# Performance work log

Hardware: AMD Instinct MI355X
Metric: run time of the kernel (lower is better)

## Reference

```python
import jax, jax.numpy as jnp
import numpy as np

B, T, DIM, HEADS = 4, 2048, 1024, 16
D_K = DIM // HEADS


def setup_inputs() -> dict:
    key = jax.random.key(0)
    ks = jax.random.split(key, 5)
    x = jax.random.normal(ks[0], (B, T, DIM), dtype=jnp.float32)
    # nn.Linear params: weight [out, in], bias [out]
    w_qkv = jax.random.normal(ks[1], (3 * DIM, DIM), dtype=jnp.float32) / np.sqrt(DIM)
    b_qkv = jax.random.normal(ks[2], (3 * DIM,), dtype=jnp.float32) * 0.02
    w_out = jax.random.normal(ks[3], (DIM, DIM), dtype=jnp.float32) / np.sqrt(DIM)
    b_out = jax.random.normal(ks[4], (DIM,), dtype=jnp.float32) * 0.02
    # causal mask, broadcast over batch and heads: [1, 1, T, T]
    mask = jnp.tril(jnp.ones((T, T), dtype=jnp.int32))[None, None]
    return {"x": x, "w_qkv": w_qkv, "b_qkv": b_qkv, "w_out": w_out, "b_out": b_out, "mask": mask}


def reference(x, w_qkv, b_qkv, w_out, b_out, mask):
    Bb, Tt, D = x.shape
    # fused QKV projection: [B,T,3D] -> [3,B,H,T,d_k]
    qkv = (x @ w_qkv.T + b_qkv).reshape(Bb, Tt, 3, HEADS, D_K).transpose(2, 0, 3, 1, 4)
    q, k, v = qkv[0], qkv[1], qkv[2]
    scores = jnp.einsum("bhqd,bhkd->bhqk", q, k) / jnp.sqrt(jnp.float32(D_K))
    scores = jnp.where(mask == 0, -jnp.inf, scores)
    attn = jax.nn.softmax(scores, axis=-1)  # [B,H,T,T]
    context = jnp.einsum("bhqk,bhkd->bhqd", attn, v)
    context = context.transpose(0, 2, 1, 3).reshape(Bb, Tt, D)
    return context @ w_out.T + b_out
```

## Files before the change

kernel.cpp:

```cpp
#include <hip/hip_runtime.h>

typedef unsigned short ushort_t;
typedef __bf16 bf16x8 __attribute__((ext_vector_type(8)));
typedef float f32x4 __attribute__((ext_vector_type(4)));

#define BB 4
#define TT 2048
#define DIMD 1024
#define NH 16
#define DK 64
#define MROWS (BB * TT)
#define NQKV (3 * DIMD)

__device__ __forceinline__ ushort_t f2b(float f) {
  __bf16 h = (__bf16)f;
  union { __bf16 h; ushort_t u; } c; c.h = h; return c.u;
}
__device__ __forceinline__ float fexp2(float x) {
  float r;
  asm("v_exp_f32 %0, %1" : "=v"(r) : "v"(x));
  return r;
}

__device__ __forceinline__ void gload_lds16(const void* g, void* l) {
  __builtin_amdgcn_global_load_lds(
      (const __attribute__((address_space(1))) void*)g,
      (__attribute__((address_space(3))) void*)l,
      16, 0, 0);
}

__global__ __launch_bounds__(256) void cast_f32_bf16(
    const float* __restrict__ in, ushort_t* __restrict__ out, int n)
{
  const int i = (blockIdx.x * 256 + threadIdx.x) * 8;
  if (i >= n) return;
  float4 a = *(const float4*)(in + i);
  float4 b = *(const float4*)(in + i + 4);
  ushort_t o[8];
  o[0] = f2b(a.x); o[1] = f2b(a.y); o[2] = f2b(a.z); o[3] = f2b(a.w);
  o[4] = f2b(b.x); o[5] = f2b(b.y); o[6] = f2b(b.z); o[7] = f2b(b.w);
  *(uint4*)(out + i) = *(const uint4*)o;
}

template <bool OUT_F32>
__global__ __launch_bounds__(512, 4) void gemm_bt_pipe(
    const ushort_t* __restrict__ A, const ushort_t* __restrict__ W,
    const float* __restrict__ bias, void* __restrict__ Cp,
    int M, int N, int K)
{
  __shared__ __align__(16) ushort_t As[3][128 * 32];
  __shared__ __align__(16) ushort_t Bs[3][256 * 32];

  const int tid = threadIdx.x;
  const int wave = tid >> 6, lane = tid & 63;
  const int x = blockIdx.x & 7, j = blockIdx.x >> 3;
  const int bm = (x << 3) | (j & 7);
  const int bn = j >> 3;
  const int row0 = bm << 7, col0 = bn << 8;
  const int wm = (wave >> 2) << 6;
  const int wn = (wave & 3) << 6;
  const int fr = lane & 15;
  const int g  = lane >> 4;
  const int g4 = g << 2;
  const int csw = (g ^ (fr >> 2)) << 3;

  const int srow = lane >> 2;
  const int scol = ((lane & 3) ^ ((lane >> 4) & 3)) << 3;
  const int lbase = wave << 9;

  const ushort_t* Ag  = A + (size_t)(row0 + (wave << 4) + srow) * K + scol;
  const ushort_t* Wg0 = W + (size_t)(col0 + (wave << 4) + srow) * K + scol;
  const ushort_t* Wg1 = Wg0 + (size_t)128 * K;

#define STAGE_P(kt, buf)                                                      \
  {                                                                           \
    const size_t _k = (size_t)(kt) << 5;                                      \
    gload_lds16(Ag + _k,  &As[buf][lbase]);                                   \
    gload_lds16(Wg0 + _k, &Bs[buf][lbase]);                                   \
    gload_lds16(Wg1 + _k, &Bs[buf][4096 + lbase]);                            \
  }

  const int NT = K >> 5;
  STAGE_P(0, 0);
  STAGE_P(1, 1);

  f32x4 acc[4][4] = {};
  int cr = 0, st = 2;

  for (int t = 0; t < NT; ++t) {
    if (t + 1 < NT) asm volatile("s_waitcnt vmcnt(3)" ::: "memory");
    else            asm volatile("s_waitcnt vmcnt(0)" ::: "memory");
    __builtin_amdgcn_s_barrier();

    const ushort_t* as_ = As[cr];
    const ushort_t* bs_ = Bs[cr];
    bf16x8 af0 = *(const bf16x8*)&as_[(wm +      fr) * 32 + csw];
    bf16x8 af1 = *(const bf16x8*)&as_[(wm + 16 + fr) * 32 + csw];
    bf16x8 bw0 = *(const bf16x8*)&bs_[(wn +      fr) * 32 + csw];
    bf16x8 bw1 = *(const bf16x8*)&bs_[(wn + 16 + fr) * 32 + csw];
    bf16x8 bw2 = *(const bf16x8*)&bs_[(wn + 32 + fr) * 32 + csw];
    bf16x8 bw3 = *(const bf16x8*)&bs_[(wn + 48 + fr) * 32 + csw];
    if (t + 2 < NT) STAGE_P(t + 2, st);
    asm volatile("s_waitcnt lgkmcnt(0)" ::: "memory");
    __builtin_amdgcn_sched_barrier(0);
    __builtin_amdgcn_s_setprio(1);
    acc[0][0] = __builtin_amdgcn_mfma_f32_16x16x32_bf16(af0, bw0, acc[0][0], 0, 0, 0);
    acc[0][1] = __builtin_amdgcn_mfma_f32_16x16x32_bf16(af0, bw1, acc[0][1], 0, 0, 0);
    acc[0][2] = __builtin_amdgcn_mfma_f32_16x16x32_bf16(af0, bw2, acc[0][2], 0, 0, 0);
    acc[0][3] = __builtin_amdgcn_mfma_f32_16x16x32_bf16(af0, bw3, acc[0][3], 0, 0, 0);
    acc[1][0] = __builtin_amdgcn_mfma_f32_16x16x32_bf16(af1, bw0, acc[1][0], 0, 0, 0);
    acc[1][1] = __builtin_amdgcn_mfma_f32_16x16x32_bf16(af1, bw1, acc[1][1], 0, 0, 0);
    acc[1][2] = __builtin_amdgcn_mfma_f32_16x16x32_bf16(af1, bw2, acc[1][2], 0, 0, 0);
    acc[1][3] = __builtin_amdgcn_mfma_f32_16x16x32_bf16(af1, bw3, acc[1][3], 0, 0, 0);
    __builtin_amdgcn_s_setprio(0);

    bf16x8 af2 = *(const bf16x8*)&as_[(wm + 32 + fr) * 32 + csw];
    bf16x8 af3 = *(const bf16x8*)&as_[(wm + 48 + fr) * 32 + csw];
    asm volatile("s_waitcnt lgkmcnt(0)" ::: "memory");
    __builtin_amdgcn_sched_barrier(0);
    __builtin_amdgcn_s_setprio(1);
    acc[2][0] = __builtin_amdgcn_mfma_f32_16x16x32_bf16(af2, bw0, acc[2][0], 0, 0, 0);
    acc[2][1] = __builtin_amdgcn_mfma_f32_16x16x32_bf16(af2, bw1, acc[2][1], 0, 0, 0);
    acc[2][2] = __builtin_amdgcn_mfma_f32_16x16x32_bf16(af2, bw2, acc[2][2], 0, 0, 0);
    acc[2][3] = __builtin_amdgcn_mfma_f32_16x16x32_bf16(af2, bw3, acc[2][3], 0, 0, 0);
    acc[3][0] = __builtin_amdgcn_mfma_f32_16x16x32_bf16(af3, bw0, acc[3][0], 0, 0, 0);
    acc[3][1] = __builtin_amdgcn_mfma_f32_16x16x32_bf16(af3, bw1, acc[3][1], 0, 0, 0);
    acc[3][2] = __builtin_amdgcn_mfma_f32_16x16x32_bf16(af3, bw2, acc[3][2], 0, 0, 0);
    acc[3][3] = __builtin_amdgcn_mfma_f32_16x16x32_bf16(af3, bw3, acc[3][3], 0, 0, 0);
    __builtin_amdgcn_s_setprio(0);

    ++cr; if (cr == 3) cr = 0;
    ++st; if (st == 3) st = 0;
  }
#undef STAGE_P

#pragma unroll
  for (int jj = 0; jj < 4; ++jj) {
    const int col = col0 + wn + (jj << 4) + fr;
    const float bv = bias[col];
#pragma unroll
    for (int i = 0; i < 4; ++i)
#pragma unroll
      for (int r = 0; r < 4; ++r) {
        const size_t row = (size_t)(row0 + wm + (i << 4) + g4 + r);
        if constexpr (OUT_F32)
          ((float*)Cp)[row * (size_t)N + col] = acc[i][jj][r] + bv;
        else
          ((ushort_t*)Cp)[row * (size_t)N + col] = f2b(acc[i][jj][r] + bv);
      }
  }
}

#define C1 0.18033688011112042f
__global__ __launch_bounds__(512, 4) void attn_fused(
    const ushort_t* __restrict__ qkv, ushort_t* __restrict__ ctx)
{
  __shared__ __align__(16) ushort_t Qs[128 * 64];
  __shared__ __align__(16) ushort_t Ks[2][64 * 64];
  __shared__ __align__(16) ushort_t Vt[2][64 * 64];
  __shared__ __align__(16) ushort_t Ps[8][16 * 64];

  const int tid = threadIdx.x, wave = tid >> 6, lane = tid & 63;
  const int fr = lane & 15;
  const int g  = lane >> 4;
  const int fk = g << 3;
  const int g4 = g << 2;

  const int bid = blockIdx.x;
  const int bq  = (bid >> 3) & 7;
  const int G   = (bid & 7) | ((bid >> 6) << 3);
  const int h   = G & 15;
  const int b   = G >> 4;

  const int srl = lane >> 3;
  const int scc = ((lane & 7) ^ srl) << 3;
  const int vr  = tid >> 3;
  const int vc  = (tid & 7) << 3;
  const int rsw = (fr & 7) << 3;

  const ushort_t* Kg = qkv + (size_t)b * TT * NQKV + DIMD + h * DK;
  const ushort_t* Vg = qkv + (size_t)b * TT * NQKV + 2 * DIMD + h * DK;

#pragma unroll 1
  for (int t = 0; t < 2; ++t) {
    const int qt = t ? (15 - bq) : bq;
    const int ktmax = 2 * qt + 1;
    const int diag  = 2 * qt + (wave >> 2);
    const size_t qrow0 = (size_t)b * TT + (size_t)qt * 128;

    __syncthreads();

    const ushort_t* Qg = qkv + qrow0 * NQKV + h * DK;
    uint4 va = *(const uint4*)(Vg + (size_t)vr * NQKV + vc);
#pragma unroll
    for (int pp = 0; pp < 2; ++pp) {
      const int e  = (wave << 9) + (pp << 12);
      const int rr = (e >> 6) + srl;
      gload_lds16(Qg + (size_t)rr * NQKV + scc, Qs + e);
    }
    {
      const int e  = wave << 9;
      const int rr = (wave << 3) + srl;
      gload_lds16(Kg + (size_t)rr * NQKV + scc, Ks[0] + e);
    }
    asm volatile("s_waitcnt vmcnt(0)" ::: "memory");
    __syncthreads();

    bf16x8 aqr[2];
#pragma unroll
    for (int ks = 0; ks < 2; ++ks)
      aqr[ks] = *(const bf16x8*)&Qs[((wave << 4) + fr) * 64 + (((ks << 5) + fk) ^ rsw)];

    {
      __align__(16) ushort_t tmp[8];
      *(uint4*)tmp = va;
#pragma unroll
      for (int jj = 0; jj < 8; ++jj) {
        const int d  = vc + jj;
        const int hh = (d & 7) ^ ((d >> 3) & 7);
        Vt[0][d * 64 + (vr ^ (hh << 3))] = tmp[jj];
      }
    }
    va = *(const uint4*)(Vg + (size_t)(64 + vr) * NQKV + vc);
    asm volatile("s_waitcnt lgkmcnt(0)" ::: "memory");

    const int qrow = (qt << 7) + (wave << 4) + fr;
    float mrow = -1e30f, lrow = 0.f;
    f32x4 oacc[4] = {};

    for (int kt = 0; kt <= ktmax; ++kt) {
      asm volatile("s_waitcnt vmcnt(0)" ::: "memory");
      __builtin_amdgcn_s_barrier();

      const int cur = kt & 1, nxt = cur ^ 1;
      f32x4 s[4];

      if (kt <= diag) {
#pragma unroll
        for (int ni = 0; ni < 4; ++ni) s[ni] = f32x4{0.f, 0.f, 0.f, 0.f};
        __builtin_amdgcn_s_setprio(1);
#pragma unroll
        for (int ks = 0; ks < 2; ++ks)
#pragma unroll
          for (int ni = 0; ni < 4; ++ni) {
            const bf16x8 bk = *(const bf16x8*)&Ks[cur][((ni << 4) + fr) * 64 + (((ks << 5) + fk) ^ rsw)];
            s[ni] = __builtin_amdgcn_mfma_f32_16x16x32_bf16(bk, aqr[ks], s[ni], 0, 0, 0);
          }
        __builtin_amdgcn_s_setprio(0);
      }

      if (kt < ktmax) {
        const size_t krow = (size_t)(kt + 1) << 6;
        const int e  = wave << 9;
        const int rr = (wave << 3) + srl;
        gload_lds16(Kg + (krow + rr) * NQKV + scc, Ks[nxt] + e);
        {
          __align__(16) ushort_t tmp[8];
          *(uint4*)tmp = va;
#pragma unroll
          for (int jj = 0; jj < 8; ++jj) {
            const int d  = vc + jj;
            const int hh = (d & 7) ^ ((d >> 3) & 7);
            Vt[nxt][d * 64 + (vr ^ (hh << 3))] = tmp[jj];
          }
        }
        if (kt + 1 < ktmax)
          va = *(const uint4*)(Vg + ((size_t)(kt + 2) * 64 + vr) * NQKV + vc);
      }

      if (kt <= diag) {
        if (kt == diag) {
          const int kb = kt << 6;
#pragma unroll
          for (int ni = 0; ni < 4; ++ni)
#pragma unroll
            for (int r = 0; r < 4; ++r) {
              const int kc = kb + (ni << 4) + g4 + r;
              if (kc > qrow) s[ni][r] = -1e30f;
            }
        }

        float rm = -1e30f;
#pragma unroll
        for (int ni = 0; ni < 4; ++ni) {
          const float m01 = fmaxf(s[ni][0], s[ni][1]);
          const float m23 = fmaxf(s[ni][2], s[ni][3]);
          rm = fmaxf(rm, fmaxf(m01, m23));
        }
        rm = fmaxf(rm, __shfl_xor(rm, 16, 64));
        rm = fmaxf(rm, __shfl_xor(rm, 32, 64));

        if (__any(rm > mrow + 64.f)) {
          const float mn = fmaxf(mrow, rm);
          const float corr = fexp2((mrow - mn) * C1);
          mrow = mn;
          lrow *= corr;
#pragma unroll
          for (int ni = 0; ni < 4; ++ni) oacc[ni] *= corr;
        }
        const float nm2 = -mrow * C1;
        float rs = 0.f;
#pragma unroll
        for (int ni = 0; ni < 4; ++ni)
#pragma unroll
          for (int r = 0; r < 4; ++r) {
            const float pe = fexp2(fmaf(s[ni][r], C1, nm2));
            s[ni][r] = pe;
            rs += pe;
          }
        rs += __shfl_xor(rs, 16, 64);
        rs += __shfl_xor(rs, 32, 64);
        lrow += rs;

#pragma unroll
        for (int ni = 0; ni < 4; ++ni) {
          ushort_t o4[4];
#pragma unroll
          for (int r = 0; r < 4; ++r) o4[r] = f2b(s[ni][r]);
          *(uint2*)&Ps[wave][fr * 64 + (((ni << 4) + g4) ^ rsw)] = *(const uint2*)o4;
        }
        asm volatile("s_waitcnt lgkmcnt(0)" ::: "memory");
        __builtin_amdgcn_sched_barrier(0);

        __builtin_amdgcn_s_setprio(1);
#pragma unroll
        for (int ks = 0; ks < 2; ++ks) {
          const bf16x8 ap = *(const bf16x8*)&Ps[wave][fr * 64 + (((ks << 5) + fk) ^ rsw)];
#pragma unroll
          for (int ni = 0; ni < 4; ++ni) {
            const int hh = (fr & 7) ^ ((2 * ni + (fr >> 3)) & 7);
            const bf16x8 bv = *(const bf16x8*)&Vt[cur][((ni << 4) + fr) * 64 + (((ks << 5) + fk) ^ (hh << 3))];
            oacc[ni] = __builtin_amdgcn_mfma_f32_16x16x32_bf16(bv, ap, oacc[ni], 0, 0, 0);
          }
        }
        __builtin_amdgcn_s_setprio(0);
      }

      asm volatile("s_waitcnt lgkmcnt(0)" ::: "memory");
    }

    const float inv = 1.f / lrow;
    ushort_t* crow = ctx + (qrow0 + (wave << 4) + fr) * DIMD + h * DK;
#pragma unroll
    for (int ni = 0; ni < 4; ++ni) {
      ushort_t o4[4];
#pragma unroll
      for (int r = 0; r < 4; ++r) o4[r] = f2b(oacc[ni][r] * inv);
      *(uint2*)&crow[(ni << 4) + g4] = *(const uint2*)o4;
    }
  }
}

extern "C" void kernel_launch(void* const* d_in, const int* in_sizes, int n_in,
                              void* d_out, int out_size, void* d_ws, size_t ws_size,
                              hipStream_t stream) {
  const float* x     = (const float*)d_in[0];
  const float* w_qkv = (const float*)d_in[1];
  const float* b_qkv = (const float*)d_in[2];
  const float* w_out = (const float*)d_in[3];
  const float* b_out = (const float*)d_in[4];

  const size_t need = 36u * 1024 * 1024 * sizeof(ushort_t);
  if (ws_size < need) return;

  ushort_t* qkv = (ushort_t*)d_ws;
  ushort_t* xb  = qkv + (size_t)MROWS * NQKV;
  ushort_t* wqb = xb  + (size_t)MROWS * DIMD;
  ushort_t* wob = wqb + (size_t)NQKV * DIMD;
  ushort_t* ctx = xb;
  float*    out = (float*)d_out;

  cast_f32_bf16<<<dim3(MROWS * DIMD / 2048), dim3(256), 0, stream>>>(x, xb, MROWS * DIMD);
  cast_f32_bf16<<<dim3(NQKV * DIMD / 2048), dim3(256), 0, stream>>>(w_qkv, wqb, NQKV * DIMD);
  cast_f32_bf16<<<dim3(DIMD * DIMD / 2048), dim3(256), 0, stream>>>(w_out, wob, DIMD * DIMD);
  gemm_bt_pipe<false><<<dim3((MROWS / 128) * (NQKV / 256)), dim3(512), 0, stream>>>(
      xb, wqb, b_qkv, (void*)qkv, MROWS, NQKV, DIMD);
  attn_fused<<<dim3(BB * NH * 8), dim3(512), 0, stream>>>(qkv, ctx);
  gemm_bt_pipe<true><<<dim3((MROWS / 128) * (DIMD / 256)), dim3(512), 0, stream>>>(
      ctx, wob, b_out, (void*)out, MROWS, DIMD, DIMD);
}
```

Baseline: 182.5 us.

## Shrink attention LDS, one q-tile per block, new output-projection GEMM

The attention kernel stops pairing two query tiles per block. It launches one block per 128-row query tile, ordered longest-first, and raises the occupancy hint to 8 blocks per CU. LDS is cut by single-buffering V^T and aliasing the Q staging buffer with the V^T/P region, at the cost of an extra barrier per key step. V is now written into LDS before the next K/V loads are issued. The output projection switches to a new, simpler 128x128-tile, 256-thread GEMM without the old pipelining, which adds tail imbalance and loses load overlap in exchange for more blocks.

```diff
diff --git a/kernel.cpp b/kernel.cpp
--- a/kernel.cpp
+++ b/kernel.cpp
@@ -151,14 +151,82 @@
   }
 }
 
+template <bool OUT_F32>
+__global__ __launch_bounds__(256) void gemm_bt_bias(
+    const ushort_t* __restrict__ A, const ushort_t* __restrict__ W,
+    const float* __restrict__ bias, void* __restrict__ Cp,
+    int M, int N, int K)
+{
+  __shared__ __align__(16) ushort_t As[128 * 32];
+  __shared__ __align__(16) ushort_t Bs[128 * 32];
+
+  const int tid = threadIdx.x;
+  const int wave = tid >> 6, lane = tid & 63;
+  const int tiles_n = N >> 7;
+  const int bm = blockIdx.x / tiles_n, bn = blockIdx.x % tiles_n;
+  const int row0 = bm << 7, col0 = bn << 7;
+  const int wm = (wave >> 1) << 6;
+  const int wn = (wave & 1) << 6;
+  const int fr = lane & 15;
+  const int fk = (lane >> 4) << 3;
+  const int g4 = (lane >> 4) << 2;
+
+  const int sr = lane >> 2;
+  const int csw = fk ^ (((fr >> 1) & 3) << 3);
+
+  f32x4 acc[4][4] = {};
+
+  for (int k0 = 0; k0 < K; k0 += 32) {
+    __syncthreads();
+#pragma unroll
+    for (int p = 0; p < 2; ++p) {
+      const int e = (wave << 9) + (p << 11);
+      const int r = (e >> 5) + sr;
+      const int c = ((lane & 3) << 3) ^ (((r >> 1) & 3) << 3);
+      gload_lds16(A + (size_t)(row0 + r) * K + (k0 + c), As + e);
+      gload_lds16(W + (size_t)(col0 + r) * K + (k0 + c), Bs + e);
+    }
+    __syncthreads();
+
+    bf16x8 af[4], bw[4];
+#pragma unroll
+    for (int i = 0; i < 4; ++i) {
+      af[i] = *(const bf16x8*)&As[(wm + (i << 4) + fr) * 32 + csw];
+      bw[i] = *(const bf16x8*)&Bs[(wn + (i << 4) + fr) * 32 + csw];
+    }
+#pragma unroll
+    for (int mi = 0; mi < 4; ++mi)
+#pragma unroll
+      for (int ni = 0; ni < 4; ++ni)
+        acc[mi][ni] = __builtin_amdgcn_mfma_f32_16x16x32_bf16(af[mi], bw[ni], acc[mi][ni], 0, 0, 0);
+  }
+
+#pragma unroll
+  for (int ni = 0; ni < 4; ++ni) {
+    const int col = col0 + wn + (ni << 4) + fr;
+    const float bv = bias[col];
+#pragma unroll
+    for (int mi = 0; mi < 4; ++mi)
+#pragma unroll
+      for (int r = 0; r < 4; ++r) {
+        const size_t row = (size_t)(row0 + wm + (mi << 4) + g4 + r);
+        if constexpr (OUT_F32)
+          ((float*)Cp)[row * (size_t)N + col] = acc[mi][ni][r] + bv;
+        else
+          ((ushort_t*)Cp)[row * (size_t)N + col] = f2b(acc[mi][ni][r] + bv);
+      }
+  }
+}
+
 #define C1 0.18033688011112042f
-__global__ __launch_bounds__(512, 4) void attn_fused(
+__global__ __launch_bounds__(512, 8) void attn_fused(
     const ushort_t* __restrict__ qkv, ushort_t* __restrict__ ctx)
 {
-  __shared__ __align__(16) ushort_t Qs[128 * 64];
   __shared__ __align__(16) ushort_t Ks[2][64 * 64];
-  __shared__ __align__(16) ushort_t Vt[2][64 * 64];
-  __shared__ __align__(16) ushort_t Ps[8][16 * 64];
+  __shared__ __align__(16) ushort_t U[12288];
+  ushort_t* const Vt = U;
+  ushort_t* const Ps = U + 4096;
+  ushort_t* const Qs = U;
 
   const int tid = threadIdx.x, wave = tid >> 6, lane = tid & 63;
   const int fr = lane & 15;
@@ -167,8 +235,8 @@
   const int g4 = g << 2;
 
   const int bid = blockIdx.x;
-  const int bq  = (bid >> 3) & 7;
-  const int G   = (bid & 7) | ((bid >> 6) << 3);
+  const int qt  = 15 - ((bid >> 3) & 15);
+  const int G   = (bid & 7) | ((bid >> 7) << 3);
   const int h   = G & 15;
   const int b   = G >> 4;
 
@@ -181,36 +249,38 @@
   const ushort_t* Kg = qkv + (size_t)b * TT * NQKV + DIMD + h * DK;
   const ushort_t* Vg = qkv + (size_t)b * TT * NQKV + 2 * DIMD + h * DK;
 
-#pragma unroll 1
-  for (int t = 0; t < 2; ++t) {
-    const int qt = t ? (15 - bq) : bq;
-    const int ktmax = 2 * qt + 1;
-    const int diag  = 2 * qt + (wave >> 2);
-    const size_t qrow0 = (size_t)b * TT + (size_t)qt * 128;
-
-    __syncthreads();
-
-    const ushort_t* Qg = qkv + qrow0 * NQKV + h * DK;
-    uint4 va = *(const uint4*)(Vg + (size_t)vr * NQKV + vc);
-#pragma unroll
-    for (int pp = 0; pp < 2; ++pp) {
-      const int e  = (wave << 9) + (pp << 12);
-      const int rr = (e >> 6) + srl;
-      gload_lds16(Qg + (size_t)rr * NQKV + scc, Qs + e);
-    }
-    {
-      const int e  = wave << 9;
-      const int rr = (wave << 3) + srl;
-      gload_lds16(Kg + (size_t)rr * NQKV + scc, Ks[0] + e);
-    }
-    asm volatile("s_waitcnt vmcnt(0)" ::: "memory");
-    __syncthreads();
-
-    bf16x8 aqr[2];
-#pragma unroll
-    for (int ks = 0; ks < 2; ++ks)
-      aqr[ks] = *(const bf16x8*)&Qs[((wave << 4) + fr) * 64 + (((ks << 5) + fk) ^ rsw)];
-
+  const int ktmax = 2 * qt + 1;
+  const int diag  = 2 * qt + (wave >> 2);
+  const size_t qrow0 = (size_t)b * TT + (size_t)qt * 128;
+
+  const ushort_t* Qg = qkv + qrow0 * NQKV + h * DK;
+  uint4 va = *(const uint4*)(Vg + (size_t)vr * NQKV + vc);
+#pragma unroll
+  for (int pp = 0; pp < 2; ++pp) {
+    const int e  = (wave << 9) + (pp << 12);
+    const int rr = (e >> 6) + srl;
+    gload_lds16(Qg + (size_t)rr * NQKV + scc, Qs + e);
+  }
+  {
+    const int e  = wave << 9;
+    const int rr = (wave << 3) + srl;
+    gload_lds16(Kg + (size_t)rr * NQKV + scc, Ks[0] + e);
+  }
+  asm volatile("s_waitcnt vmcnt(0)" ::: "memory");
+  __syncthreads();
+
+  bf16x8 aqr[2];
+#pragma unroll
+  for (int ks = 0; ks < 2; ++ks)
+    aqr[ks] = *(const bf16x8*)&Qs[((wave << 4) + fr) * 64 + (((ks << 5) + fk) ^ rsw)];
+  __syncthreads();
+
+  const int qrow = (qt << 7) + (wave << 4) + fr;
+  float mrow = -1e30f, lrow = 0.f;
+  f32x4 oacc[4] = {};
+  int cur = 0;
+
+  for (int kt = 0; kt <= ktmax; ++kt) {
     {
       __align__(16) ushort_t tmp[8];
       *(uint4*)tmp = va;
@@ -218,136 +288,113 @@
       for (int jj = 0; jj < 8; ++jj) {
         const int d  = vc + jj;
         const int hh = (d & 7) ^ ((d >> 3) & 7);
-        Vt[0][d * 64 + (vr ^ (hh << 3))] = tmp[jj];
-      }
-    }
-    va = *(const uint4*)(Vg + (size_t)(64 + vr) * NQKV + vc);
+        Vt[d * 64 + (vr ^ (hh << 3))] = tmp[jj];
+      }
+    }
+    if (kt < ktmax) {
+      const size_t krow = (size_t)(kt + 1) << 6;
+      const int e  = wave << 9;
+      const int rr = (wave << 3) + srl;
+      gload_lds16(Kg + (krow + rr) * NQKV + scc, Ks[cur ^ 1] + e);
+      va = *(const uint4*)(Vg + (krow + vr) * NQKV + vc);
+    }
     asm volatile("s_waitcnt lgkmcnt(0)" ::: "memory");
-
-    const int qrow = (qt << 7) + (wave << 4) + fr;
-    float mrow = -1e30f, lrow = 0.f;
-    f32x4 oacc[4] = {};
-
-    for (int kt = 0; kt <= ktmax; ++kt) {
+    __builtin_amdgcn_s_barrier();
+
+    if (kt <= diag) {
+      f32x4 s[4] = {};
+      __builtin_amdgcn_s_setprio(1);
+#pragma unroll
+      for (int ks = 0; ks < 2; ++ks)
+#pragma unroll
+        for (int ni = 0; ni < 4; ++ni) {
+          const bf16x8 bk = *(const bf16x8*)&Ks[cur][((ni << 4) + fr) * 64 + (((ks << 5) + fk) ^ rsw)];
+          s[ni] = __builtin_amdgcn_mfma_f32_16x16x32_bf16(bk, aqr[ks], s[ni], 0, 0, 0);
+        }
+      __builtin_amdgcn_s_setprio(0);
+
+      if (kt == diag) {
+        const int kb = kt << 6;
+#pragma unroll
+        for (int ni = 0; ni < 4; ++ni)
+#pragma unroll
+          for (int r = 0; r < 4; ++r) {
+            const int kc = kb + (ni << 4) + g4 + r;
+            if (kc > qrow) s[ni][r] = -1e30f;
+          }
+      }
+
+      float rm = -1e30f;
+#pragma unroll
+      for (int ni = 0; ni < 4; ++ni) {
+        const float m01 = fmaxf(s[ni][0], s[ni][1]);
+        const float m23 = fmaxf(s[ni][2], s[ni][3]);
+        rm = fmaxf(rm, fmaxf(m01, m23));
+      }
+      rm = fmaxf(rm, __shfl_xor(rm, 16, 64));
+      rm = fmaxf(rm, __shfl_xor(rm, 32, 64));
+
+      if (__any(rm > mrow + 64.f)) {
+        const float mn = fmaxf(mrow, rm);
+        const float corr = fexp2((mrow - mn) * C1);
+        mrow = mn;
+        lrow *= corr;
+#pragma unroll
+        for (int ni = 0; ni < 4; ++ni) oacc[ni] *= corr;
+      }
+      const float nm2 = -mrow * C1;
+      float rs = 0.f;
+#pragma unroll
+      for (int ni = 0; ni < 4; ++ni)
+#pragma unroll
+        for (int r = 0; r < 4; ++r) {
+          const float pe = fexp2(fmaf(s[ni][r], C1, nm2));
+          s[ni][r] = pe;
+          rs += pe;
+        }
+      rs += __shfl_xor(rs, 16, 64);
+      rs += __shfl_xor(rs, 32, 64);
+      lrow += rs;
+
+#pragma unroll
+      for (int ni = 0; ni < 4; ++ni) {
+        ushort_t o4[4];
+#pragma unroll
+        for (int r = 0; r < 4; ++r) o4[r] = f2b(s[ni][r]);
+        *(uint2*)&Ps[(wave << 10) + fr * 64 + (((ni << 4) + g4) ^ rsw)] = *(const uint2*)o4;
+      }
+      asm volatile("s_waitcnt lgkmcnt(0)" ::: "memory");
+      __builtin_amdgcn_sched_barrier(0);
+
+      __builtin_amdgcn_s_setprio(1);
+#pragma unroll
+      for (int ks = 0; ks < 2; ++ks) {
+        const bf16x8 ap = *(const bf16x8*)&Ps[(wave << 10) + fr * 64 + (((ks << 5) + fk) ^ rsw)];
+#pragma unroll
+        for (int ni = 0; ni < 4; ++ni) {
+          const int hh = (fr & 7) ^ ((2 * ni + (fr >> 3)) & 7);
+          const bf16x8 bv = *(const bf16x8*)&Vt[((ni << 4) + fr) * 64 + (((ks << 5) + fk) ^ (hh << 3))];
+          oacc[ni] = __builtin_amdgcn_mfma_f32_16x16x32_bf16(bv, ap, oacc[ni], 0, 0, 0);
+        }
+      }
+      __builtin_amdgcn_s_setprio(0);
+    }
+
+    if (kt < ktmax) {
       asm volatile("s_waitcnt vmcnt(0)" ::: "memory");
-      __builtin_amdgcn_s_barrier();
-
-      const int cur = kt & 1, nxt = cur ^ 1;
-      f32x4 s[4];
-
-      if (kt <= diag) {
-#pragma unroll
-        for (int ni = 0; ni < 4; ++ni) s[ni] = f32x4{0.f, 0.f, 0.f, 0.f};
-        __builtin_amdgcn_s_setprio(1);
-#pragma unroll
-        for (int ks = 0; ks < 2; ++ks)
-#pragma unroll
-          for (int ni = 0; ni < 4; ++ni) {
-            const bf16x8 bk = *(const bf16x8*)&Ks[cur][((ni << 4) + fr) * 64 + (((ks << 5) + fk) ^ rsw)];
-            s[ni] = __builtin_amdgcn_mfma_f32_16x16x32_bf16(bk, aqr[ks], s[ni], 0, 0, 0);
-          }
-        __builtin_amdgcn_s_setprio(0);
-      }
-
-      if (kt < ktmax) {
-        const size_t krow = (size_t)(kt + 1) << 6;
-        const int e  = wave << 9;
-        const int rr = (wave << 3) + srl;
-        gload_lds16(Kg + (krow + rr) * NQKV + scc, Ks[nxt] + e);
-        {
-          __align__(16) ushort_t tmp[8];
-          *(uint4*)tmp = va;
-#pragma unroll
-          for (int jj = 0; jj < 8; ++jj) {
-            const int d  = vc + jj;
-            const int hh = (d & 7) ^ ((d >> 3) & 7);
-            Vt[nxt][d * 64 + (vr ^ (hh << 3))] = tmp[jj];
-          }
-        }
-        if (kt + 1 < ktmax)
-          va = *(const uint4*)(Vg + ((size_t)(kt + 2) * 64 + vr) * NQKV + vc);
-      }
-
-      if (kt <= diag) {
-        if (kt == diag) {
-          const int kb = kt << 6;
-#pragma unroll
-          for (int ni = 0; ni < 4; ++ni)
-#pragma unroll
-            for (int r = 0; r < 4; ++r) {
-              const int kc = kb + (ni << 4) + g4 + r;
-              if (kc > qrow) s[ni][r] = -1e30f;
-            }
-        }
-
-        float rm = -1e30f;
-#pragma unroll
-        for (int ni = 0; ni < 4; ++ni) {
-          const float m01 = fmaxf(s[ni][0], s[ni][1]);
-          const float m23 = fmaxf(s[ni][2], s[ni][3]);
-          rm = fmaxf(rm, fmaxf(m01, m23));
-        }
-        rm = fmaxf(rm, __shfl_xor(rm, 16, 64));
-        rm = fmaxf(rm, __shfl_xor(rm, 32, 64));
-
-        if (__any(rm > mrow + 64.f)) {
-          const float mn = fmaxf(mrow, rm);
-          const float corr = fexp2((mrow - mn) * C1);
-          mrow = mn;
-          lrow *= corr;
-#pragma unroll
-          for (int ni = 0; ni < 4; ++ni) oacc[ni] *= corr;
-        }
-        const float nm2 = -mrow * C1;
-        float rs = 0.f;
-#pragma unroll
-        for (int ni = 0; ni < 4; ++ni)
-#pragma unroll
-          for (int r = 0; r < 4; ++r) {
-            const float pe = fexp2(fmaf(s[ni][r], C1, nm2));
-            s[ni][r] = pe;
-            rs += pe;
-          }
-        rs += __shfl_xor(rs, 16, 64);
-        rs += __shfl_xor(rs, 32, 64);
-        lrow += rs;
-
-#pragma unroll
-        for (int ni = 0; ni < 4; ++ni) {
-          ushort_t o4[4];
-#pragma unroll
-          for (int r = 0; r < 4; ++r) o4[r] = f2b(s[ni][r]);
-          *(uint2*)&Ps[wave][fr * 64 + (((ni << 4) + g4) ^ rsw)] = *(const uint2*)o4;
-        }
-        asm volatile("s_waitcnt lgkmcnt(0)" ::: "memory");
-        __builtin_amdgcn_sched_barrier(0);
-
-        __builtin_amdgcn_s_setprio(1);
-#pragma unroll
-        for (int ks = 0; ks < 2; ++ks) {
-          const bf16x8 ap = *(const bf16x8*)&Ps[wave][fr * 64 + (((ks << 5) + fk) ^ rsw)];
-#pragma unroll
-          for (int ni = 0; ni < 4; ++ni) {
-            const int hh = (fr & 7) ^ ((2 * ni + (fr >> 3)) & 7);
-            const bf16x8 bv = *(const bf16x8*)&Vt[cur][((ni << 4) + fr) * 64 + (((ks << 5) + fk) ^ (hh << 3))];
-            oacc[ni] = __builtin_amdgcn_mfma_f32_16x16x32_bf16(bv, ap, oacc[ni], 0, 0, 0);
-          }
-        }
-        __builtin_amdgcn_s_setprio(0);
-      }
-
-      asm volatile("s_waitcnt lgkmcnt(0)" ::: "memory");
-    }
-
-    const float inv = 1.f / lrow;
-    ushort_t* crow = ctx + (qrow0 + (wave << 4) + fr) * DIMD + h * DK;
-#pragma unroll
-    for (int ni = 0; ni < 4; ++ni) {
-      ushort_t o4[4];
-#pragma unroll
-      for (int r = 0; r < 4; ++r) o4[r] = f2b(oacc[ni][r] * inv);
-      *(uint2*)&crow[(ni << 4) + g4] = *(const uint2*)o4;
-    }
+      __syncthreads();
+    }
+    cur ^= 1;
+  }
+
+  const float inv = 1.f / lrow;
+  ushort_t* crow = ctx + (qrow0 + (wave << 4) + fr) * DIMD + h * DK;
+#pragma unroll
+  for (int ni = 0; ni < 4; ++ni) {
+    ushort_t o4[4];
+#pragma unroll
+    for (int r = 0; r < 4; ++r) o4[r] = f2b(oacc[ni][r] * inv);
+    *(uint2*)&crow[(ni << 4) + g4] = *(const uint2*)o4;
   }
 }
 
@@ -375,7 +422,7 @@
   cast_f32_bf16<<<dim3(DIMD * DIMD / 2048), dim3(256), 0, stream>>>(w_out, wob, DIMD * DIMD);
   gemm_bt_pipe<false><<<dim3((MROWS / 128) * (NQKV / 256)), dim3(512), 0, stream>>>(
       xb, wqb, b_qkv, (void*)qkv, MROWS, NQKV, DIMD);
-  attn_fused<<<dim3(BB * NH * 8), dim3(512), 0, stream>>>(qkv, ctx);
-  gemm_bt_pipe<true><<<dim3((MROWS / 128) * (DIMD / 256)), dim3(512), 0, stream>>>(
+  attn_fused<<<dim3(BB * NH * 16), dim3(512), 0, stream>>>(qkv, ctx);
+  gemm_bt_bias<true><<<dim3((MROWS / 128) * (DIMD / 128)), dim3(256), 0, stream>>>(
       ctx, wob, b_out, (void*)out, MROWS, DIMD, DIMD);
 }
```

After: 323.5 us. 1.77x slower.
